# Kernel optimization log

Hardware: AMD Instinct MI355X
Metric: run time of the kernel (lower is better)

Reference implementation:

```python
import jax, jax.numpy as jnp
import numpy as np

N, D = 4096, 512
TAU, ALPHA, BETA = 0.8, 0.55, 0.4
ADJ_P = 0.005  # sparse binary adjacency density (avg degree ~20)


def setup_inputs() -> dict:
    key = jax.random.key(0)
    ks = jax.random.split(key, 8)
    z1 = jax.random.normal(ks[0], (N, D), dtype=jnp.float32)
    z2 = jax.random.normal(ks[1], (N, D), dtype=jnp.float32)

    def adj(k):
        a = jax.random.bernoulli(k, ADJ_P, (N, N)).astype(jnp.float32)
        # adjacency masks are binary {0,1}; zero the diagonal like the model does
        return a * (1.0 - jnp.eye(N, dtype=jnp.float32))

    return {
        "z1": z1,
        "z2": z2,
        "adj_c": adj(ks[2]),
        "adj_m": adj(ks[3]),
        "adj_f": adj(ks[4]),
        "adj_c_aug": adj(ks[5]),
        "adj_m_aug": adj(ks[6]),
        "adj_f_aug": adj(ks[7]),
    }


def _normalize(z):
    # F.normalize(z, dim=1): divide by L2 norm clamped at 1e-12
    n = jnp.maximum(jnp.linalg.norm(z, axis=1, keepdims=True), 1e-12)
    return z / n


def _cl_loss(z, z_aug, adj, tau):
    zn = _normalize(z)
    zan = _normalize(z_aug)
    intra = jnp.exp((zn @ zn.T) / tau)          # [N, N]
    inter = jnp.exp((zn @ zan.T) / tau)         # [N, N]
    intra_diag = jnp.diagonal(intra)
    positive = jnp.diagonal(inter) + (intra * adj).sum(1) + (inter * adj).sum(1)
    denom = intra.sum(1) + inter.sum(1) - intra_diag
    adj_count = adj.sum(1) * 2.0 + 1.0
    loss = jnp.log(positive / denom) / adj_count
    return -jnp.mean(loss)


def _final_cl_loss(z, z_aug, adj, adj_aug, tau):
    return ALPHA * _cl_loss(z, z_aug, adj, tau) + BETA * _cl_loss(z_aug, z, adj_aug, tau)


def reference(z1, z2, adj_c, adj_m, adj_f, adj_c_aug, adj_m_aug, adj_f_aug):
    loss_coarse = _final_cl_loss(z1, z2, adj_c, adj_c_aug, TAU)
    loss_medium = _final_cl_loss(z1, z2, adj_m, adj_m_aug, TAU)
    loss_fine = _final_cl_loss(z1, z2, adj_f, adj_f_aug, TAU)
    loss_cross_cf = _final_cl_loss(z1, z2, adj_c, adj_f_aug, TAU * 0.8)
    loss_cross_mf = _final_cl_loss(z1, z2, adj_m, adj_f_aug, TAU * 0.9)

    sc, sm, sf = adj_c.sum(), adj_m.sum(), adj_f.sum()
    total_info = sc + sm + sf + 1e-08
    scale_loss = (sc / total_info) * loss_coarse + (sm / total_info) * loss_medium + (sf / total_info) * loss_fine
    cross_loss = 0.2 * (loss_cross_cf + loss_cross_mf)
    return scale_loss + cross_loss
```

## Files before the change

kernel.cpp:

```cpp
#include <hip/hip_runtime.h>
#include <hip/hip_bf16.h>

#define NR 4096
#define DD 512
#define CAP 64

typedef __bf16 bf16x8 __attribute__((ext_vector_type(8)));
typedef float f32x4 __attribute__((ext_vector_type(4)));
typedef unsigned short u16;

#define AS_GLOBAL(p) ((const __attribute__((address_space(1))) unsigned int*)(p))
#define AS_LDS(p)    ((__attribute__((address_space(3))) unsigned int*)(p))

__device__ __forceinline__ u16 f2bf(float x) {
    __hip_bfloat16 h = __float2bfloat16(x);
    return *reinterpret_cast<u16*>(&h);
}

__device__ __forceinline__ float blo(unsigned u) { return __uint_as_float(u << 16); }
__device__ __forceinline__ float bhi(unsigned u) { return __uint_as_float(u & 0xffff0000u); }

__global__ void norm_kernel(const float* z1, const float* z2,
                            u16* zn1, u16* zn2, float* d12) {
    const int row = blockIdx.x;
    const int t = threadIdx.x;
    const float* r1 = z1 + (size_t)row * DD;
    const float* r2 = z2 + (size_t)row * DD;
    float a0 = r1[t], a1 = r1[t + 256];
    float b0 = r2[t], b1 = r2[t + 256];
    float ss1 = a0 * a0 + a1 * a1;
    float ss2 = b0 * b0 + b1 * b1;
    #pragma unroll
    for (int m = 1; m < 64; m <<= 1) {
        ss1 += __shfl_xor(ss1, m);
        ss2 += __shfl_xor(ss2, m);
    }
    __shared__ float s1s[4], s2s[4], ds[4];
    const int wid = t >> 6, lane = t & 63;
    if (lane == 0) { s1s[wid] = ss1; s2s[wid] = ss2; }
    __syncthreads();
    const float n1 = s1s[0] + s1s[1] + s1s[2] + s1s[3];
    const float n2 = s2s[0] + s2s[1] + s2s[2] + s2s[3];
    const float inv1 = 1.0f / fmaxf(sqrtf(n1), 1e-12f);
    const float inv2 = 1.0f / fmaxf(sqrtf(n2), 1e-12f);
    const float u0 = a0 * inv1, u1 = a1 * inv1;
    const float v0 = b0 * inv2, v1 = b1 * inv2;
    zn1[(size_t)row * DD + t]       = f2bf(u0);
    zn1[(size_t)row * DD + t + 256] = f2bf(u1);
    zn2[(size_t)row * DD + t]       = f2bf(v0);
    zn2[(size_t)row * DD + t + 256] = f2bf(v1);
    float dp = u0 * v0 + u1 * v1;
    #pragma unroll
    for (int m = 1; m < 64; m <<= 1) dp += __shfl_xor(dp, m);
    if (lane == 0) ds[wid] = dp;
    __syncthreads();
    if (t == 0) d12[row] = ds[0] + ds[1] + ds[2] + ds[3];
}

__global__ __launch_bounds__(256, 2)
void fused_kernel(const u16* __restrict__ zn1, const u16* __restrict__ zn2,
                  const float* __restrict__ m0, const float* __restrict__ m1,
                  const float* __restrict__ m2, const float* __restrict__ m3,
                  const float* __restrict__ m4, const float* __restrict__ m5,
                  float* __restrict__ part, float* __restrict__ ms,
                  float* __restrict__ asum) {
    __shared__ u16 As[128 * 64];
    __shared__ u16 Bs[128 * 64];
    __shared__ float sRow[2][3][128];
    __shared__ float sCol[2][3][128];

    const int bid = blockIdx.x;
    const int tid = threadIdx.x;
    const int lane = tid & 63;

    const float C0 = 1.8033688011112042f;
    const float C1 = 2.2542110013890054f;
    const float C2 = 2.0037431123457825f;

    if ((bid & 3) == 0) {
        int id = bid >> 2;
        int mode, by, bx;
        if (id < 1024) {
            mode = 1; by = id >> 5; bx = id & 31;
        } else {
            int k = id - 1024;
            mode = 0;
            if (k >= 528) { k -= 528; mode = 2; }
            int v = (int)((65.0f - sqrtf(4225.0f - 8.0f * (float)k)) * 0.5f);
            if (v < 0) v = 0; if (v > 31) v = 31;
            while (v < 31 && (v + 1) * 32 - ((v + 1) * v) / 2 <= k) v++;
            while (v > 0 && v * 32 - (v * (v - 1)) / 2 > k) v--;
            by = v;
            bx = by + (k - (by * 32 - (by * (by - 1)) / 2));
        }
        const int Ib = by * 128, Jb = bx * 128;
        const u16* Ag = (mode == 2) ? zn2 : zn1;
        const u16* Bg = (mode == 0) ? zn1 : zn2;
        const int p_row = mode;
        const int p_col = (mode == 1) ? 3 : mode;
        const bool do_cols = (mode == 1) || (bx != by);

        const int wid = tid >> 6;
        const int wm = wid >> 1, wn = wid & 1;
        const int quad = lane >> 4, lcol = lane & 15;

        f32x4 acc[4][4];
        #pragma unroll
        for (int a = 0; a < 4; a++)
            #pragma unroll
            for (int b = 0; b < 4; b++)
                acc[a][b] = (f32x4){0.f, 0.f, 0.f, 0.f};

        size_t gA[4], gB[4];
        unsigned ldsoff[4];
        #pragma unroll
        for (int cc = 0; cc < 4; cc++) {
            const int ch = cc * 4 + wid;
            const int p = ch * 64 + lane;
            const int r = p >> 3;
            const int kb = (p & 7) ^ (r & 7);
            ldsoff[cc] = (unsigned)ch * 1024u;
            gA[cc] = (size_t)(Ib + r) * DD + kb * 8;
            gB[cc] = (size_t)(Jb + r) * DD + kb * 8;
        }

        for (int k0 = 0; k0 < DD; k0 += 64) {
            __syncthreads();
            #pragma unroll
            for (int cc = 0; cc < 4; cc++) {
                __builtin_amdgcn_global_load_lds(AS_GLOBAL(Ag + gA[cc] + k0),
                                                 AS_LDS((char*)As + ldsoff[cc]), 16, 0, 0);
                __builtin_amdgcn_global_load_lds(AS_GLOBAL(Bg + gB[cc] + k0),
                                                 AS_LDS((char*)Bs + ldsoff[cc]), 16, 0, 0);
            }
            __syncthreads();
            #pragma unroll
            for (int kk = 0; kk < 64; kk += 32) {
                const int kbb = (kk >> 3) + quad;
                bf16x8 a[4], b[4];
                #pragma unroll
                for (int i = 0; i < 4; i++) {
                    const int ra = wm * 64 + i * 16 + lcol;
                    const int rb = wn * 64 + i * 16 + lcol;
                    a[i] = *(const bf16x8*)&As[ra * 64 + ((kbb ^ (ra & 7)) * 8)];
                    b[i] = *(const bf16x8*)&Bs[rb * 64 + ((kbb ^ (rb & 7)) * 8)];
                }
                #pragma unroll
                for (int mi = 0; mi < 4; mi++)
                    #pragma unroll
                    for (int ni = 0; ni < 4; ni++)
                        acc[mi][ni] = __builtin_amdgcn_mfma_f32_16x16x32_bf16(a[mi], b[ni], acc[mi][ni], 0, 0, 0);
            }
        }

        float colacc[3][4];
        #pragma unroll
        for (int t = 0; t < 3; t++)
            #pragma unroll
            for (int ni = 0; ni < 4; ni++) colacc[t][ni] = 0.f;

        #pragma unroll
        for (int mi = 0; mi < 4; mi++) {
            #pragma unroll
            for (int reg = 0; reg < 4; reg++) {
                float p0 = 0.f, p1 = 0.f, p2 = 0.f;
                #pragma unroll
                for (int ni = 0; ni < 4; ni++) {
                    const float s = acc[mi][ni][reg];
                    const float e0 = __builtin_amdgcn_exp2f(s * C0);
                    const float e1 = __builtin_amdgcn_exp2f(s * C1);
                    const float e2 = __builtin_amdgcn_exp2f(s * C2);
                    p0 += e0; p1 += e1; p2 += e2;
                    colacc[0][ni] += e0; colacc[1][ni] += e1; colacc[2][ni] += e2;
                }
                p0 += __shfl_xor(p0, 1); p0 += __shfl_xor(p0, 2); p0 += __shfl_xor(p0, 4); p0 += __shfl_xor(p0, 8);
                p1 += __shfl_xor(p1, 1); p1 += __shfl_xor(p1, 2); p1 += __shfl_xor(p1, 4); p1 += __shfl_xor(p1, 8);
                p2 += __shfl_xor(p2, 1); p2 += __shfl_xor(p2, 2); p2 += __shfl_xor(p2, 4); p2 += __shfl_xor(p2, 8);
                if (lcol == 0) {
                    const int r = wm * 64 + mi * 16 + quad * 4 + reg;
                    sRow[wn][0][r] = p0; sRow[wn][1][r] = p1; sRow[wn][2][r] = p2;
                }
            }
        }
        #pragma unroll
        for (int t = 0; t < 3; t++) {
            #pragma unroll
            for (int ni = 0; ni < 4; ni++) {
                float v = colacc[t][ni];
                v += __shfl_xor(v, 16); v += __shfl_xor(v, 32);
                if (quad == 0) sCol[wm][t][wn * 64 + ni * 16 + lcol] = v;
            }
        }
        __syncthreads();
        if (tid < 128) {
            const int i = Ib + tid;
            #pragma unroll
            for (int t = 0; t < 3; t++) {
                const float v = sRow[0][t][tid] + sRow[1][t][tid];
                part[(((size_t)p_row * 3 + t) * 32 + bx) * NR + i] = v;
            }
        } else if (do_cols) {
            const int c = tid - 128;
            const int i = Jb + c;
            #pragma unroll
            for (int t = 0; t < 3; t++) {
                const float v = sCol[0][t][c] + sCol[1][t][c];
                part[(((size_t)p_col * 3 + t) * 32 + by) * NR + i] = v;
            }
        }
    } else {
        const int sid = bid - (bid >> 2) - 1;
        if (sid >= 6144) return;
        const int widx = tid >> 6;
        const int w = sid * 4 + widx;
        const int g = lane >> 4;
        const int l = lane & 15;
        const int m = w >> 12;
        const int i = w & (NR - 1);

        const float* M = (m == 0) ? m0 : (m == 1) ? m1 : (m == 2) ? m2
                       : (m == 3) ? m3 : (m == 4) ? m4 : m5;
        const float4* p = (const float4*)(M + (size_t)i * NR) + lane;
        unsigned long long mask = 0ull;
        #pragma unroll
        for (int t = 0; t < 16; t++) {
            const float4 v = p[t * 64];
            mask |= (unsigned long long)((v.x != 0.f ? 1u : 0u)
                   | (v.y != 0.f ? 2u : 0u)
                   | (v.z != 0.f ? 4u : 0u)
                   | (v.w != 0.f ? 8u : 0u)) << (t * 4);
        }
        const int n = __popcll(mask);
        int off = n;
        #pragma unroll
        for (int d = 1; d < 64; d <<= 1) {
            const int tu = __shfl_up(off, d);
            if (lane >= d) off += tu;
        }
        const int total = __shfl(off, 63);
        int pos = off - n;
        int* lidx = ((int*)As) + widx * 64;
        unsigned long long mm = mask;
        while (mm) {
            const int b = __ffsll(mm) - 1;
            mm &= mm - 1;
            if (pos < CAP) lidx[pos] = ((b >> 2) * 64 + lane) * 4 + (b & 3);
            pos++;
        }
        if (lane == 63) asum[(size_t)m * NR + i] = (float)total;
        const int cnt = min(total, CAP);
        __syncthreads();
        const int jreg = lidx[lane];

        int nslot; int slot[3]; float coef[3];
        switch (m) {
            case 0: nslot = 2; slot[0] = 0; coef[0] = C0; slot[1] = 3; coef[1] = C1; break;
            case 1: nslot = 2; slot[0] = 1; coef[0] = C0; slot[1] = 4; coef[1] = C2; break;
            case 2: nslot = 1; slot[0] = 2; coef[0] = C0; break;
            case 3: nslot = 1; slot[0] = 0; coef[0] = C0; break;
            case 4: nslot = 1; slot[0] = 1; coef[0] = C0; break;
            default: nslot = 3; slot[0] = 2; coef[0] = C0; slot[1] = 3; coef[1] = C1;
                     slot[2] = 4; coef[2] = C2; break;
        }

        const u16* A = (m < 3) ? zn1 : zn2;
        unsigned au[16];
        {
            const uint4* ap = (const uint4*)(A + (size_t)i * DD) + l * 4;
            #pragma unroll
            for (int t = 0; t < 4; t++) {
                const uint4 r = ap[t];
                au[t * 4 + 0] = r.x; au[t * 4 + 1] = r.y;
                au[t * 4 + 2] = r.z; au[t * 4 + 3] = r.w;
            }
        }

        float acc[3][2] = {{0.f, 0.f}, {0.f, 0.f}, {0.f, 0.f}};

        for (int q0 = 0; q0 < cnt; q0 += 8) {
            const int qa = q0 + g;
            const int qb = qa + 4;
            const bool va = qa < cnt;
            const bool vb = qb < cnt;
            const int ja = __shfl(jreg, va ? qa : 0);
            const int jb = __shfl(jreg, vb ? qb : 0);

            const uint4* p1a = (const uint4*)(zn1 + (size_t)ja * DD) + l * 4;
            const uint4* p2a = (const uint4*)(zn2 + (size_t)ja * DD) + l * 4;
            const uint4* p1b = (const uint4*)(zn1 + (size_t)jb * DD) + l * 4;
            const uint4* p2b = (const uint4*)(zn2 + (size_t)jb * DD) + l * 4;
            uint4 r1a[4], r2a[4], r1b[4], r2b[4];
            #pragma unroll
            for (int t = 0; t < 4; t++) {
                r1a[t] = p1a[t]; r2a[t] = p2a[t];
                r1b[t] = p1b[t]; r2b[t] = p2b[t];
            }

            float s1a0 = 0.f, s1a1 = 0.f, s2a0 = 0.f, s2a1 = 0.f;
            float s1b0 = 0.f, s1b1 = 0.f, s2b0 = 0.f, s2b1 = 0.f;
            #pragma unroll
            for (int t = 0; t < 4; t++) {
                const unsigned* u1a = (const unsigned*)&r1a[t];
                const unsigned* u2a = (const unsigned*)&r2a[t];
                const unsigned* u1b = (const unsigned*)&r1b[t];
                const unsigned* u2b = (const unsigned*)&r2b[t];
                #pragma unroll
                for (int q = 0; q < 4; q++) {
                    const unsigned aw = au[t * 4 + q];
                    const float alo = blo(aw), ahi = bhi(aw);
                    s1a0 += alo * blo(u1a[q]); s1a1 += ahi * bhi(u1a[q]);
                    s2a0 += alo * blo(u2a[q]); s2a1 += ahi * bhi(u2a[q]);
                    s1b0 += alo * blo(u1b[q]); s1b1 += ahi * bhi(u1b[q]);
                    s2b0 += alo * blo(u2b[q]); s2b1 += ahi * bhi(u2b[q]);
                }
            }
            float d1a = s1a0 + s1a1, d2a = s2a0 + s2a1;
            float d1b = s1b0 + s1b1, d2b = s2b0 + s2b1;

            #pragma unroll
            for (int msk = 1; msk < 16; msk <<= 1) {
                d1a += __shfl_xor(d1a, msk); d2a += __shfl_xor(d2a, msk);
                d1b += __shfl_xor(d1b, msk); d2b += __shfl_xor(d2b, msk);
            }

            const float e1a = (m < 3) ? d1a : d2a, e2a = (m < 3) ? d2a : d1a;
            const float e1b = (m < 3) ? d1b : d2b, e2b = (m < 3) ? d2b : d1b;
            if (va) {
                for (int s = 0; s < nslot; s++) {
                    acc[s][0] += __builtin_amdgcn_exp2f(e1a * coef[s]);
                    acc[s][1] += __builtin_amdgcn_exp2f(e2a * coef[s]);
                }
            }
            if (vb) {
                for (int s = 0; s < nslot; s++) {
                    acc[s][0] += __builtin_amdgcn_exp2f(e1b * coef[s]);
                    acc[s][1] += __builtin_amdgcn_exp2f(e2b * coef[s]);
                }
            }
        }

        #pragma unroll
        for (int s = 0; s < 3; s++) {
            #pragma unroll
            for (int h = 0; h < 2; h++) {
                float v = acc[s][h];
                v += __shfl_xor(v, 16);
                v += __shfl_xor(v, 32);
                acc[s][h] = v;
            }
        }
        if (lane == 0) {
            const int pb = (m < 3) ? 0 : 2;
            for (int s = 0; s < nslot; s++) {
                ms[((pb)     * 5 + slot[s]) * NR + i] = acc[s][0];
                ms[((pb + 1) * 5 + slot[s]) * NR + i] = acc[s][1];
            }
        }
    }
}

__global__ __launch_bounds__(256)
void reduce_kernel(const float* __restrict__ part, float* __restrict__ rs) {
    const int g = blockIdx.x * 256 + threadIdx.x;
    const int pt = g >> 12;
    const int i = g & (NR - 1);
    const float* base = part + ((size_t)pt * 32) * NR + i;
    float s = 0.f;
    #pragma unroll
    for (int k = 0; k < 32; k++) s += base[(size_t)k * NR];
    rs[(size_t)pt * NR + i] = s;
}

__global__ void finalize_kernel(const float* rs, const float* ms, const float* asum,
                                const float* d12, float* out) {
    const int t = threadIdx.x;
    const int tA[5] = {0, 0, 0, 1, 2};
    const int kA[5] = {0, 1, 2, 3, 4};
    const int aA[5] = {0, 1, 2, 0, 1};
    const int aB[5] = {3, 4, 5, 5, 5};
    const float it[3] = {1.25f, 1.5625f, 1.3888888888888888f};
    const float e1t[3] = {expf(1.25f), expf(1.5625f), expf(1.3888888888888888f)};

    float LA[5] = {0, 0, 0, 0, 0}, LB[5] = {0, 0, 0, 0, 0};
    float sc = 0.f, sm = 0.f, sf = 0.f;

    for (int i = t; i < NR; i += 256) {
        const float d = d12[i];
        float ed[3];
        ed[0] = __expf(d * it[0]); ed[1] = __expf(d * it[1]); ed[2] = __expf(d * it[2]);
        float R[4][3], M[4][5], A6[6];
        #pragma unroll
        for (int p = 0; p < 4; p++) {
            #pragma unroll
            for (int tt = 0; tt < 3; tt++) R[p][tt] = rs[(p * 3 + tt) * NR + i];
            #pragma unroll
            for (int k = 0; k < 5; k++) M[p][k] = ms[(p * 5 + k) * NR + i];
        }
        #pragma unroll
        for (int a = 0; a < 6; a++) A6[a] = asum[a * NR + i];

        #pragma unroll
        for (int c = 0; c < 5; c++) {
            const int tt = tA[c], k = kA[c];
            float pos = ed[tt] + M[0][k] + M[1][k];
            float den = R[0][tt] + R[1][tt] - e1t[tt];
            float cnt = 2.f * A6[aA[c]] + 1.f;
            LA[c] += __logf(pos / den) / cnt;
            pos = ed[tt] + M[2][k] + M[3][k];
            den = R[2][tt] + R[3][tt] - e1t[tt];
            cnt = 2.f * A6[aB[c]] + 1.f;
            LB[c] += __logf(pos / den) / cnt;
        }
        sc += A6[0]; sm += A6[1]; sf += A6[2];
    }

    __shared__ float red[256];
    float vals[13] = {LA[0], LA[1], LA[2], LA[3], LA[4],
                      LB[0], LB[1], LB[2], LB[3], LB[4], sc, sm, sf};
    __shared__ float tot[13];
    for (int q = 0; q < 13; q++) {
        red[t] = vals[q];
        __syncthreads();
        for (int s = 128; s > 0; s >>= 1) {
            if (t < s) red[t] += red[t + s];
            __syncthreads();
        }
        if (t == 0) tot[q] = red[0];
        __syncthreads();
    }
    if (t == 0) {
        float Ac[5], Bc[5];
        #pragma unroll
        for (int c = 0; c < 5; c++) {
            Ac[c] = -tot[c] / (float)NR;
            Bc[c] = -tot[5 + c] / (float)NR;
        }
        const float ALPHA = 0.55f, BETA = 0.4f;
        const float Lc  = ALPHA * Ac[0] + BETA * Bc[0];
        const float Lm  = ALPHA * Ac[1] + BETA * Bc[1];
        const float Lf  = ALPHA * Ac[2] + BETA * Bc[2];
        const float Lcf = ALPHA * Ac[3] + BETA * Bc[3];
        const float Lmf = ALPHA * Ac[4] + BETA * Bc[4];
        const float scs = tot[10], sms = tot[11], sfs = tot[12];
        const float tot_info = scs + sms + sfs + 1e-8f;
        out[0] = (scs * Lc + sms * Lm + sfs * Lf) / tot_info + 0.2f * (Lcf + Lmf);
    }
}

extern "C" void kernel_launch(void* const* d_in, const int* in_sizes, int n_in,
                              void* d_out, int out_size, void* d_ws, size_t ws_size,
                              hipStream_t stream) {
    const float* z1  = (const float*)d_in[0];
    const float* z2  = (const float*)d_in[1];
    const float* ac  = (const float*)d_in[2];
    const float* am  = (const float*)d_in[3];
    const float* af  = (const float*)d_in[4];
    const float* aca = (const float*)d_in[5];
    const float* ama = (const float*)d_in[6];
    const float* afa = (const float*)d_in[7];

    float* ws   = (float*)d_ws;
    float* rs   = ws;
    float* ms   = rs + 12 * NR;
    float* asum = ms + 20 * NR;
    float* d12  = asum + 6 * NR;
    u16* zn1 = (u16*)(d12 + NR);
    u16* zn2 = zn1 + (size_t)NR * DD;
    float* part = (float*)(zn2 + (size_t)NR * DD);

    norm_kernel<<<NR, 256, 0, stream>>>(z1, z2, zn1, zn2, d12);
    fused_kernel<<<8320, 256, 0, stream>>>(zn1, zn2, ac, am, af, aca, ama, afa,
                                           part, ms, asum);
    reduce_kernel<<<12 * NR / 256, 256, 0, stream>>>(part, rs);
    finalize_kernel<<<1, 256, 0, stream>>>(rs, ms, asum, d12, (float*)d_out);
}
```

Measured before the change: 534.1 us.

## Share A tile across two B operands per GEMM block with triangular tiling

Each GEMM block now loads one A tile and two B tiles (zn1 and zn2), computing both the intra and inter similarity tiles in one pass over upper-triangular tile pairs. The inter products are covered by transposed column sums, and the sRow/sCol scratch reuses the A tile's LDS. This cuts A-tile loads and block count from 2080 to 1056 GEMM blocks, and the interleave ratio with the sparse-mask blocks changes from 1:3 to 1:6. It doubles accumulator registers to 128 floats, which may cause spills or lower occupancy under launch_bounds(256,2).

```diff
diff --git a/kernel.cpp b/kernel.cpp
--- a/kernel.cpp
+++ b/kernel.cpp
@@ -65,9 +65,8 @@
                   float* __restrict__ part, float* __restrict__ ms,
                   float* __restrict__ asum) {
     __shared__ u16 As[128 * 64];
-    __shared__ u16 Bs[128 * 64];
-    __shared__ float sRow[2][3][128];
-    __shared__ float sCol[2][3][128];
+    __shared__ u16 Bs1[128 * 64];
+    __shared__ u16 Bs2[128 * 64];
 
     const int bid = blockIdx.x;
     const int tid = threadIdx.x;
@@ -77,39 +76,40 @@
     const float C1 = 2.2542110013890054f;
     const float C2 = 2.0037431123457825f;
 
-    if ((bid & 3) == 0) {
-        int id = bid >> 2;
-        int mode, by, bx;
-        if (id < 1024) {
-            mode = 1; by = id >> 5; bx = id & 31;
-        } else {
-            int k = id - 1024;
-            mode = 0;
-            if (k >= 528) { k -= 528; mode = 2; }
-            int v = (int)((65.0f - sqrtf(4225.0f - 8.0f * (float)k)) * 0.5f);
-            if (v < 0) v = 0; if (v > 31) v = 31;
-            while (v < 31 && (v + 1) * 32 - ((v + 1) * v) / 2 <= k) v++;
-            while (v > 0 && v * 32 - (v * (v - 1)) / 2 > k) v--;
-            by = v;
-            bx = by + (k - (by * 32 - (by * (by - 1)) / 2));
-        }
+    const int q7 = bid / 7;
+    if (bid - q7 * 7 == 0) {
+        const int id = q7;
+        const int grp = id & 1;
+        int k = id >> 1;
+        int v = (int)((65.0f - sqrtf(4225.0f - 8.0f * (float)k)) * 0.5f);
+        if (v < 0) v = 0; if (v > 31) v = 31;
+        while (v < 31 && (v + 1) * 32 - ((v + 1) * v) / 2 <= k) v++;
+        while (v > 0 && v * 32 - (v * (v - 1)) / 2 > k) v--;
+        const int by = v;
+        const int bx = by + (k - (by * 32 - (by * (by - 1)) / 2));
+
         const int Ib = by * 128, Jb = bx * 128;
-        const u16* Ag = (mode == 2) ? zn2 : zn1;
-        const u16* Bg = (mode == 0) ? zn1 : zn2;
-        const int p_row = mode;
-        const int p_col = (mode == 1) ? 3 : mode;
-        const bool do_cols = (mode == 1) || (bx != by);
+        const bool diag = (bx == by);
+        const u16* Ag  = grp ? zn2 : zn1;
+        const u16* B1g = grp ? zn2 : zn1;
+        const u16* B2g = grp ? zn1 : zn2;
+        const bool dualB = !(grp == 1 && diag);
+        const int pR1 = grp ? 2 : 0;
+        const int pR2 = grp ? 3 : 1;
+        const int pC2 = grp ? 1 : 3;
 
         const int wid = tid >> 6;
         const int wm = wid >> 1, wn = wid & 1;
         const int quad = lane >> 4, lcol = lane & 15;
 
-        f32x4 acc[4][4];
+        f32x4 acc1[4][4], acc2[4][4];
         #pragma unroll
         for (int a = 0; a < 4; a++)
             #pragma unroll
-            for (int b = 0; b < 4; b++)
-                acc[a][b] = (f32x4){0.f, 0.f, 0.f, 0.f};
+            for (int b = 0; b < 4; b++) {
+                acc1[a][b] = (f32x4){0.f, 0.f, 0.f, 0.f};
+                acc2[a][b] = (f32x4){0.f, 0.f, 0.f, 0.f};
+            }
 
         size_t gA[4], gB[4];
         unsigned ldsoff[4];
@@ -130,55 +130,86 @@
             for (int cc = 0; cc < 4; cc++) {
                 __builtin_amdgcn_global_load_lds(AS_GLOBAL(Ag + gA[cc] + k0),
                                                  AS_LDS((char*)As + ldsoff[cc]), 16, 0, 0);
-                __builtin_amdgcn_global_load_lds(AS_GLOBAL(Bg + gB[cc] + k0),
-                                                 AS_LDS((char*)Bs + ldsoff[cc]), 16, 0, 0);
+                __builtin_amdgcn_global_load_lds(AS_GLOBAL(B1g + gB[cc] + k0),
+                                                 AS_LDS((char*)Bs1 + ldsoff[cc]), 16, 0, 0);
+                if (dualB)
+                    __builtin_amdgcn_global_load_lds(AS_GLOBAL(B2g + gB[cc] + k0),
+                                                     AS_LDS((char*)Bs2 + ldsoff[cc]), 16, 0, 0);
             }
             __syncthreads();
             #pragma unroll
             for (int kk = 0; kk < 64; kk += 32) {
                 const int kbb = (kk >> 3) + quad;
-                bf16x8 a[4], b[4];
+                bf16x8 a[4], b1[4], b2[4];
                 #pragma unroll
                 for (int i = 0; i < 4; i++) {
                     const int ra = wm * 64 + i * 16 + lcol;
                     const int rb = wn * 64 + i * 16 + lcol;
-                    a[i] = *(const bf16x8*)&As[ra * 64 + ((kbb ^ (ra & 7)) * 8)];
-                    b[i] = *(const bf16x8*)&Bs[rb * 64 + ((kbb ^ (rb & 7)) * 8)];
+                    a[i]  = *(const bf16x8*)&As[ra * 64 + ((kbb ^ (ra & 7)) * 8)];
+                    b1[i] = *(const bf16x8*)&Bs1[rb * 64 + ((kbb ^ (rb & 7)) * 8)];
+                    if (dualB)
+                        b2[i] = *(const bf16x8*)&Bs2[rb * 64 + ((kbb ^ (rb & 7)) * 8)];
                 }
                 #pragma unroll
                 for (int mi = 0; mi < 4; mi++)
                     #pragma unroll
-                    for (int ni = 0; ni < 4; ni++)
-                        acc[mi][ni] = __builtin_amdgcn_mfma_f32_16x16x32_bf16(a[mi], b[ni], acc[mi][ni], 0, 0, 0);
-            }
-        }
-
-        float colacc[3][4];
+                    for (int ni = 0; ni < 4; ni++) {
+                        acc1[mi][ni] = __builtin_amdgcn_mfma_f32_16x16x32_bf16(a[mi], b1[ni], acc1[mi][ni], 0, 0, 0);
+                        if (dualB)
+                            acc2[mi][ni] = __builtin_amdgcn_mfma_f32_16x16x32_bf16(a[mi], b2[ni], acc2[mi][ni], 0, 0, 0);
+                    }
+            }
+        }
+
+        float* eb = (float*)As;
+        float* sRow1 = eb;
+        float* sRow2 = eb + 768;
+        float* sCol1 = eb + 1536;
+        float* sCol2 = eb + 2304;
+        __syncthreads();
+
+        float ca1[3][4], ca2[3][4];
         #pragma unroll
         for (int t = 0; t < 3; t++)
             #pragma unroll
-            for (int ni = 0; ni < 4; ni++) colacc[t][ni] = 0.f;
+            for (int ni = 0; ni < 4; ni++) { ca1[t][ni] = 0.f; ca2[t][ni] = 0.f; }
 
         #pragma unroll
         for (int mi = 0; mi < 4; mi++) {
             #pragma unroll
             for (int reg = 0; reg < 4; reg++) {
-                float p0 = 0.f, p1 = 0.f, p2 = 0.f;
+                float p10 = 0.f, p11 = 0.f, p12 = 0.f;
+                float p20 = 0.f, p21 = 0.f, p22 = 0.f;
                 #pragma unroll
                 for (int ni = 0; ni < 4; ni++) {
-                    const float s = acc[mi][ni][reg];
-                    const float e0 = __builtin_amdgcn_exp2f(s * C0);
-                    const float e1 = __builtin_amdgcn_exp2f(s * C1);
-                    const float e2 = __builtin_amdgcn_exp2f(s * C2);
-                    p0 += e0; p1 += e1; p2 += e2;
-                    colacc[0][ni] += e0; colacc[1][ni] += e1; colacc[2][ni] += e2;
-                }
-                p0 += __shfl_xor(p0, 1); p0 += __shfl_xor(p0, 2); p0 += __shfl_xor(p0, 4); p0 += __shfl_xor(p0, 8);
-                p1 += __shfl_xor(p1, 1); p1 += __shfl_xor(p1, 2); p1 += __shfl_xor(p1, 4); p1 += __shfl_xor(p1, 8);
-                p2 += __shfl_xor(p2, 1); p2 += __shfl_xor(p2, 2); p2 += __shfl_xor(p2, 4); p2 += __shfl_xor(p2, 8);
+                    const float s1 = acc1[mi][ni][reg];
+                    const float e0 = __builtin_amdgcn_exp2f(s1 * C0);
+                    const float e1 = __builtin_amdgcn_exp2f(s1 * C1);
+                    const float e2 = __builtin_amdgcn_exp2f(s1 * C2);
+                    p10 += e0; p11 += e1; p12 += e2;
+                    ca1[0][ni] += e0; ca1[1][ni] += e1; ca1[2][ni] += e2;
+                    if (dualB) {
+                        const float s2 = acc2[mi][ni][reg];
+                        const float f0 = __builtin_amdgcn_exp2f(s2 * C0);
+                        const float f1 = __builtin_amdgcn_exp2f(s2 * C1);
+                        const float f2 = __builtin_amdgcn_exp2f(s2 * C2);
+                        p20 += f0; p21 += f1; p22 += f2;
+                        ca2[0][ni] += f0; ca2[1][ni] += f1; ca2[2][ni] += f2;
+                    }
+                }
+                #pragma unroll
+                for (int msk = 1; msk < 16; msk <<= 1) {
+                    p10 += __shfl_xor(p10, msk); p11 += __shfl_xor(p11, msk); p12 += __shfl_xor(p12, msk);
+                    p20 += __shfl_xor(p20, msk); p21 += __shfl_xor(p21, msk); p22 += __shfl_xor(p22, msk);
+                }
                 if (lcol == 0) {
                     const int r = wm * 64 + mi * 16 + quad * 4 + reg;
-                    sRow[wn][0][r] = p0; sRow[wn][1][r] = p1; sRow[wn][2][r] = p2;
+                    sRow1[wn * 384 + 0 * 128 + r] = p10;
+                    sRow1[wn * 384 + 1 * 128 + r] = p11;
+                    sRow1[wn * 384 + 2 * 128 + r] = p12;
+                    sRow2[wn * 384 + 0 * 128 + r] = p20;
+                    sRow2[wn * 384 + 1 * 128 + r] = p21;
+                    sRow2[wn * 384 + 2 * 128 + r] = p22;
                 }
             }
         }
@@ -186,9 +217,14 @@
         for (int t = 0; t < 3; t++) {
             #pragma unroll
             for (int ni = 0; ni < 4; ni++) {
-                float v = colacc[t][ni];
-                v += __shfl_xor(v, 16); v += __shfl_xor(v, 32);
-                if (quad == 0) sCol[wm][t][wn * 64 + ni * 16 + lcol] = v;
+                float v1 = ca1[t][ni], v2 = ca2[t][ni];
+                v1 += __shfl_xor(v1, 16); v1 += __shfl_xor(v1, 32);
+                v2 += __shfl_xor(v2, 16); v2 += __shfl_xor(v2, 32);
+                if (quad == 0) {
+                    const int c = wn * 64 + ni * 16 + lcol;
+                    sCol1[wm * 384 + t * 128 + c] = v1;
+                    sCol2[wm * 384 + t * 128 + c] = v2;
+                }
             }
         }
         __syncthreads();
@@ -196,20 +232,30 @@
             const int i = Ib + tid;
             #pragma unroll
             for (int t = 0; t < 3; t++) {
-                const float v = sRow[0][t][tid] + sRow[1][t][tid];
-                part[(((size_t)p_row * 3 + t) * 32 + bx) * NR + i] = v;
-            }
-        } else if (do_cols) {
+                const float r1 = sRow1[t * 128 + tid] + sRow1[384 + t * 128 + tid];
+                part[(((size_t)pR1 * 3 + t) * 32 + bx) * NR + i] = r1;
+                if (dualB) {
+                    const float r2 = sRow2[t * 128 + tid] + sRow2[384 + t * 128 + tid];
+                    part[(((size_t)pR2 * 3 + t) * 32 + bx) * NR + i] = r2;
+                }
+            }
+        } else {
             const int c = tid - 128;
-            const int i = Jb + c;
+            const int j = Jb + c;
             #pragma unroll
             for (int t = 0; t < 3; t++) {
-                const float v = sCol[0][t][c] + sCol[1][t][c];
-                part[(((size_t)p_col * 3 + t) * 32 + by) * NR + i] = v;
+                if (!diag) {
+                    const float c1 = sCol1[t * 128 + c] + sCol1[384 + t * 128 + c];
+                    part[(((size_t)pR1 * 3 + t) * 32 + by) * NR + j] = c1;
+                }
+                if (dualB) {
+                    const float c2 = sCol2[t * 128 + c] + sCol2[384 + t * 128 + c];
+                    part[(((size_t)pC2 * 3 + t) * 32 + by) * NR + j] = c2;
+                }
             }
         }
     } else {
-        const int sid = bid - (bid >> 2) - 1;
+        const int sid = bid - q7 - 1;
         if (sid >= 6144) return;
         const int widx = tid >> 6;
         const int w = sid * 4 + widx;
@@ -343,10 +389,10 @@
         for (int s = 0; s < 3; s++) {
             #pragma unroll
             for (int h = 0; h < 2; h++) {
-                float v = acc[s][h];
-                v += __shfl_xor(v, 16);
-                v += __shfl_xor(v, 32);
-                acc[s][h] = v;
+                float v2 = acc[s][h];
+                v2 += __shfl_xor(v2, 16);
+                v2 += __shfl_xor(v2, 32);
+                acc[s][h] = v2;
             }
         }
         if (lane == 0) {
@@ -469,7 +515,7 @@
     float* part = (float*)(zn2 + (size_t)NR * DD);
 
     norm_kernel<<<NR, 256, 0, stream>>>(z1, z2, zn1, zn2, d12);
-    fused_kernel<<<8320, 256, 0, stream>>>(zn1, zn2, ac, am, af, aca, ama, afa,
+    fused_kernel<<<7392, 256, 0, stream>>>(zn1, zn2, ac, am, af, aca, ama, afa,
                                            part, ms, asum);
     reduce_kernel<<<12 * NR / 256, 256, 0, stream>>>(part, rs);
     finalize_kernel<<<1, 256, 0, stream>>>(rs, ms, asum, d12, (float*)d_out);
```

Measured after the change: 521.1 us. -2.4%, faster.

## Rebalance fused kernel: 2 GEMM per 3 sparse blocks, two rows per wave, more occupancy

Applied to the files above, without the earlier changes.

Changes the block interleave from one GEMM tile per four blocks to two GEMM tiles per five blocks. Each sparse wave now scans two adjacency rows at once and processes neighbors one per 16-lane group instead of two. The epilogue's row and column scratch now reuses the As shared buffer, which cuts LDS so launch bounds can ask for three blocks per SM. Aims to raise occupancy and overlap the HBM-bound mask scan with the MFMA tiles, at the cost of more register pressure and less per-wave memory-level parallelism in the gather loop.

```diff
diff --git a/kernel.cpp b/kernel.cpp
--- a/kernel.cpp
+++ b/kernel.cpp
@@ -57,7 +57,7 @@
     if (t == 0) d12[row] = ds[0] + ds[1] + ds[2] + ds[3];
 }
 
-__global__ __launch_bounds__(256, 2)
+__global__ __launch_bounds__(256, 3)
 void fused_kernel(const u16* __restrict__ zn1, const u16* __restrict__ zn2,
                   const float* __restrict__ m0, const float* __restrict__ m1,
                   const float* __restrict__ m2, const float* __restrict__ m3,
@@ -66,8 +66,6 @@
                   float* __restrict__ asum) {
     __shared__ u16 As[128 * 64];
     __shared__ u16 Bs[128 * 64];
-    __shared__ float sRow[2][3][128];
-    __shared__ float sCol[2][3][128];
 
     const int bid = blockIdx.x;
     const int tid = threadIdx.x;
@@ -77,8 +75,11 @@
     const float C1 = 2.2542110013890054f;
     const float C2 = 2.0037431123457825f;
 
-    if ((bid & 3) == 0) {
-        int id = bid >> 2;
+    const int g5 = bid / 5;
+    const int r5 = bid - g5 * 5;
+
+    if (r5 < 2) {
+        const int id = g5 * 2 + r5;
         int mode, by, bx;
         if (id < 1024) {
             mode = 1; by = id >> 5; bx = id & 31;
@@ -153,6 +154,11 @@
             }
         }
 
+        __syncthreads();
+        float* eb = (float*)As;
+        float* sRow = eb;
+        float* sCol = eb + 768;
+
         float colacc[3][4];
         #pragma unroll
         for (int t = 0; t < 3; t++)
@@ -173,12 +179,17 @@
                     p0 += e0; p1 += e1; p2 += e2;
                     colacc[0][ni] += e0; colacc[1][ni] += e1; colacc[2][ni] += e2;
                 }
-                p0 += __shfl_xor(p0, 1); p0 += __shfl_xor(p0, 2); p0 += __shfl_xor(p0, 4); p0 += __shfl_xor(p0, 8);
-                p1 += __shfl_xor(p1, 1); p1 += __shfl_xor(p1, 2); p1 += __shfl_xor(p1, 4); p1 += __shfl_xor(p1, 8);
-                p2 += __shfl_xor(p2, 1); p2 += __shfl_xor(p2, 2); p2 += __shfl_xor(p2, 4); p2 += __shfl_xor(p2, 8);
+                #pragma unroll
+                for (int msk = 1; msk < 16; msk <<= 1) {
+                    p0 += __shfl_xor(p0, msk);
+                    p1 += __shfl_xor(p1, msk);
+                    p2 += __shfl_xor(p2, msk);
+                }
                 if (lcol == 0) {
                     const int r = wm * 64 + mi * 16 + quad * 4 + reg;
-                    sRow[wn][0][r] = p0; sRow[wn][1][r] = p1; sRow[wn][2][r] = p2;
+                    sRow[wn * 384 + 0 * 128 + r] = p0;
+                    sRow[wn * 384 + 1 * 128 + r] = p1;
+                    sRow[wn * 384 + 2 * 128 + r] = p2;
                 }
             }
         }
@@ -188,7 +199,7 @@
             for (int ni = 0; ni < 4; ni++) {
                 float v = colacc[t][ni];
                 v += __shfl_xor(v, 16); v += __shfl_xor(v, 32);
-                if (quad == 0) sCol[wm][t][wn * 64 + ni * 16 + lcol] = v;
+                if (quad == 0) sCol[wm * 384 + t * 128 + wn * 64 + ni * 16 + lcol] = v;
             }
         }
         __syncthreads();
@@ -196,61 +207,80 @@
             const int i = Ib + tid;
             #pragma unroll
             for (int t = 0; t < 3; t++) {
-                const float v = sRow[0][t][tid] + sRow[1][t][tid];
+                const float v = sRow[t * 128 + tid] + sRow[384 + t * 128 + tid];
                 part[(((size_t)p_row * 3 + t) * 32 + bx) * NR + i] = v;
             }
         } else if (do_cols) {
             const int c = tid - 128;
-            const int i = Jb + c;
+            const int j = Jb + c;
             #pragma unroll
             for (int t = 0; t < 3; t++) {
-                const float v = sCol[0][t][c] + sCol[1][t][c];
-                part[(((size_t)p_col * 3 + t) * 32 + by) * NR + i] = v;
+                const float v = sCol[t * 128 + c] + sCol[384 + t * 128 + c];
+                part[(((size_t)p_col * 3 + t) * 32 + by) * NR + j] = v;
             }
         }
     } else {
-        const int sid = bid - (bid >> 2) - 1;
-        if (sid >= 6144) return;
+        const int sid = g5 * 3 + (r5 - 2);
+        if (sid >= 3072) return;
         const int widx = tid >> 6;
-        const int w = sid * 4 + widx;
-        const int g = lane >> 4;
+        const int grp = lane >> 4;
         const int l = lane & 15;
-        const int m = w >> 12;
-        const int i = w & (NR - 1);
+        const int wbase = sid * 8 + widx * 2;
+        const int m = wbase >> 12;
+        const int i0 = wbase & (NR - 1);
 
         const float* M = (m == 0) ? m0 : (m == 1) ? m1 : (m == 2) ? m2
                        : (m == 3) ? m3 : (m == 4) ? m4 : m5;
-        const float4* p = (const float4*)(M + (size_t)i * NR) + lane;
-        unsigned long long mask = 0ull;
+        const float4* p0 = (const float4*)(M + (size_t)i0 * NR) + lane;
+        const float4* p1 = (const float4*)(M + (size_t)(i0 + 1) * NR) + lane;
+        unsigned long long mask0 = 0ull, mask1 = 0ull;
         #pragma unroll
         for (int t = 0; t < 16; t++) {
-            const float4 v = p[t * 64];
-            mask |= (unsigned long long)((v.x != 0.f ? 1u : 0u)
-                   | (v.y != 0.f ? 2u : 0u)
-                   | (v.z != 0.f ? 4u : 0u)
-                   | (v.w != 0.f ? 8u : 0u)) << (t * 4);
-        }
-        const int n = __popcll(mask);
-        int off = n;
+            const float4 va = p0[t * 64];
+            const float4 vb = p1[t * 64];
+            mask0 |= (unsigned long long)((va.x != 0.f ? 1u : 0u)
+                   | (va.y != 0.f ? 2u : 0u)
+                   | (va.z != 0.f ? 4u : 0u)
+                   | (va.w != 0.f ? 8u : 0u)) << (t * 4);
+            mask1 |= (unsigned long long)((vb.x != 0.f ? 1u : 0u)
+                   | (vb.y != 0.f ? 2u : 0u)
+                   | (vb.z != 0.f ? 4u : 0u)
+                   | (vb.w != 0.f ? 8u : 0u)) << (t * 4);
+        }
+        const int n0 = __popcll(mask0), n1 = __popcll(mask1);
+        int off0 = n0, off1 = n1;
         #pragma unroll
         for (int d = 1; d < 64; d <<= 1) {
-            const int tu = __shfl_up(off, d);
-            if (lane >= d) off += tu;
-        }
-        const int total = __shfl(off, 63);
-        int pos = off - n;
-        int* lidx = ((int*)As) + widx * 64;
-        unsigned long long mm = mask;
+            const int t0 = __shfl_up(off0, d);
+            const int t1 = __shfl_up(off1, d);
+            if (lane >= d) { off0 += t0; off1 += t1; }
+        }
+        const int total0 = __shfl(off0, 63), total1 = __shfl(off1, 63);
+        int* lidx0 = ((int*)As) + widx * 128;
+        int* lidx1 = lidx0 + 64;
+        int pos = off0 - n0;
+        unsigned long long mm = mask0;
         while (mm) {
             const int b = __ffsll(mm) - 1;
             mm &= mm - 1;
-            if (pos < CAP) lidx[pos] = ((b >> 2) * 64 + lane) * 4 + (b & 3);
+            if (pos < CAP) lidx0[pos] = ((b >> 2) * 64 + lane) * 4 + (b & 3);
             pos++;
         }
-        if (lane == 63) asum[(size_t)m * NR + i] = (float)total;
-        const int cnt = min(total, CAP);
-        __syncthreads();
-        const int jreg = lidx[lane];
+        pos = off1 - n1;
+        mm = mask1;
+        while (mm) {
+            const int b = __ffsll(mm) - 1;
+            mm &= mm - 1;
+            if (pos < CAP) lidx1[pos] = ((b >> 2) * 64 + lane) * 4 + (b & 3);
+            pos++;
+        }
+        if (lane == 63) {
+            asum[(size_t)m * NR + i0]     = (float)total0;
+            asum[(size_t)m * NR + i0 + 1] = (float)total1;
+        }
+        const int cnt0 = min(total0, CAP), cnt1 = min(total1, CAP);
+        const int jreg0 = lidx0[lane];
+        const int jreg1 = lidx1[lane];
 
         int nslot; int slot[3]; float coef[3];
         switch (m) {
@@ -264,96 +294,81 @@
         }
 
         const u16* A = (m < 3) ? zn1 : zn2;
-        unsigned au[16];
-        {
-            const uint4* ap = (const uint4*)(A + (size_t)i * DD) + l * 4;
-            #pragma unroll
-            for (int t = 0; t < 4; t++) {
-                const uint4 r = ap[t];
-                au[t * 4 + 0] = r.x; au[t * 4 + 1] = r.y;
-                au[t * 4 + 2] = r.z; au[t * 4 + 3] = r.w;
-            }
-        }
-
-        float acc[3][2] = {{0.f, 0.f}, {0.f, 0.f}, {0.f, 0.f}};
-
-        for (int q0 = 0; q0 < cnt; q0 += 8) {
-            const int qa = q0 + g;
-            const int qb = qa + 4;
-            const bool va = qa < cnt;
-            const bool vb = qb < cnt;
-            const int ja = __shfl(jreg, va ? qa : 0);
-            const int jb = __shfl(jreg, vb ? qb : 0);
-
-            const uint4* p1a = (const uint4*)(zn1 + (size_t)ja * DD) + l * 4;
-            const uint4* p2a = (const uint4*)(zn2 + (size_t)ja * DD) + l * 4;
-            const uint4* p1b = (const uint4*)(zn1 + (size_t)jb * DD) + l * 4;
-            const uint4* p2b = (const uint4*)(zn2 + (size_t)jb * DD) + l * 4;
-            uint4 r1a[4], r2a[4], r1b[4], r2b[4];
-            #pragma unroll
-            for (int t = 0; t < 4; t++) {
-                r1a[t] = p1a[t]; r2a[t] = p2a[t];
-                r1b[t] = p1b[t]; r2b[t] = p2b[t];
-            }
-
-            float s1a0 = 0.f, s1a1 = 0.f, s2a0 = 0.f, s2a1 = 0.f;
-            float s1b0 = 0.f, s1b1 = 0.f, s2b0 = 0.f, s2b1 = 0.f;
-            #pragma unroll
-            for (int t = 0; t < 4; t++) {
-                const unsigned* u1a = (const unsigned*)&r1a[t];
-                const unsigned* u2a = (const unsigned*)&r2a[t];
-                const unsigned* u1b = (const unsigned*)&r1b[t];
-                const unsigned* u2b = (const unsigned*)&r2b[t];
-                #pragma unroll
-                for (int q = 0; q < 4; q++) {
-                    const unsigned aw = au[t * 4 + q];
-                    const float alo = blo(aw), ahi = bhi(aw);
-                    s1a0 += alo * blo(u1a[q]); s1a1 += ahi * bhi(u1a[q]);
-                    s2a0 += alo * blo(u2a[q]); s2a1 += ahi * bhi(u2a[q]);
-                    s1b0 += alo * blo(u1b[q]); s1b1 += ahi * bhi(u1b[q]);
-                    s2b0 += alo * blo(u2b[q]); s2b1 += ahi * bhi(u2b[q]);
-                }
-            }
-            float d1a = s1a0 + s1a1, d2a = s2a0 + s2a1;
-            float d1b = s1b0 + s1b1, d2b = s2b0 + s2b1;
-
-            #pragma unroll
-            for (int msk = 1; msk < 16; msk <<= 1) {
-                d1a += __shfl_xor(d1a, msk); d2a += __shfl_xor(d2a, msk);
-                d1b += __shfl_xor(d1b, msk); d2b += __shfl_xor(d2b, msk);
-            }
-
-            const float e1a = (m < 3) ? d1a : d2a, e2a = (m < 3) ? d2a : d1a;
-            const float e1b = (m < 3) ? d1b : d2b, e2b = (m < 3) ? d2b : d1b;
-            if (va) {
+
+        for (int rr = 0; rr < 2; rr++) {
+            const int i = i0 + rr;
+            const int cnt = rr ? cnt1 : cnt0;
+            const int jreg = rr ? jreg1 : jreg0;
+
+            unsigned au[16];
+            {
+                const uint4* ap = (const uint4*)(A + (size_t)i * DD) + l * 4;
+                #pragma unroll
+                for (int t = 0; t < 4; t++) {
+                    const uint4 r = ap[t];
+                    au[t * 4 + 0] = r.x; au[t * 4 + 1] = r.y;
+                    au[t * 4 + 2] = r.z; au[t * 4 + 3] = r.w;
+                }
+            }
+
+            float acc[3][2] = {{0.f, 0.f}, {0.f, 0.f}, {0.f, 0.f}};
+
+            for (int q0 = 0; q0 < cnt; q0 += 4) {
+                const int q = q0 + grp;
+                const bool valid = q < cnt;
+                const int j = __shfl(jreg, valid ? q : 0);
+
+                const uint4* pj1 = (const uint4*)(zn1 + (size_t)j * DD) + l * 4;
+                const uint4* pj2 = (const uint4*)(zn2 + (size_t)j * DD) + l * 4;
+                uint4 r1[4], r2[4];
+                #pragma unroll
+                for (int t = 0; t < 4; t++) { r1[t] = pj1[t]; r2[t] = pj2[t]; }
+
+                float s10 = 0.f, s11 = 0.f, s20 = 0.f, s21 = 0.f;
+                #pragma unroll
+                for (int t = 0; t < 4; t++) {
+                    const unsigned* u1 = (const unsigned*)&r1[t];
+                    const unsigned* u2 = (const unsigned*)&r2[t];
+                    #pragma unroll
+                    for (int qd = 0; qd < 4; qd++) {
+                        const unsigned aw = au[t * 4 + qd];
+                        const float alo = blo(aw), ahi = bhi(aw);
+                        s10 += alo * blo(u1[qd]); s11 += ahi * bhi(u1[qd]);
+                        s20 += alo * blo(u2[qd]); s21 += ahi * bhi(u2[qd]);
+                    }
+                }
+                float d1 = s10 + s11, d2 = s20 + s21;
+                #pragma unroll
+                for (int msk = 1; msk < 16; msk <<= 1) {
+                    d1 += __shfl_xor(d1, msk);
+                    d2 += __shfl_xor(d2, msk);
+                }
+                const float e1 = (m < 3) ? d1 : d2;
+                const float e2 = (m < 3) ? d2 : d1;
+                if (valid) {
+                    for (int s = 0; s < nslot; s++) {
+                        acc[s][0] += __builtin_amdgcn_exp2f(e1 * coef[s]);
+                        acc[s][1] += __builtin_amdgcn_exp2f(e2 * coef[s]);
+                    }
+                }
+            }
+
+            #pragma unroll
+            for (int s = 0; s < 3; s++) {
+                #pragma unroll
+                for (int h = 0; h < 2; h++) {
+                    float v = acc[s][h];
+                    v += __shfl_xor(v, 16);
+                    v += __shfl_xor(v, 32);
+                    acc[s][h] = v;
+                }
+            }
+            if (lane == 0) {
+                const int pb = (m < 3) ? 0 : 2;
                 for (int s = 0; s < nslot; s++) {
-                    acc[s][0] += __builtin_amdgcn_exp2f(e1a * coef[s]);
-                    acc[s][1] += __builtin_amdgcn_exp2f(e2a * coef[s]);
-                }
-            }
-            if (vb) {
-                for (int s = 0; s < nslot; s++) {
-                    acc[s][0] += __builtin_amdgcn_exp2f(e1b * coef[s]);
-                    acc[s][1] += __builtin_amdgcn_exp2f(e2b * coef[s]);
-                }
-            }
-        }
-
-        #pragma unroll
-        for (int s = 0; s < 3; s++) {
-            #pragma unroll
-            for (int h = 0; h < 2; h++) {
-                float v = acc[s][h];
-                v += __shfl_xor(v, 16);
-                v += __shfl_xor(v, 32);
-                acc[s][h] = v;
-            }
-        }
-        if (lane == 0) {
-            const int pb = (m < 3) ? 0 : 2;
-            for (int s = 0; s < nslot; s++) {
-                ms[((pb)     * 5 + slot[s]) * NR + i] = acc[s][0];
-                ms[((pb + 1) * 5 + slot[s]) * NR + i] = acc[s][1];
+                    ms[((pb)     * 5 + slot[s]) * NR + i] = acc[s][0];
+                    ms[((pb + 1) * 5 + slot[s]) * NR + i] = acc[s][1];
+                }
             }
         }
     }
@@ -469,7 +484,7 @@
     float* part = (float*)(zn2 + (size_t)NR * DD);
 
     norm_kernel<<<NR, 256, 0, stream>>>(z1, z2, zn1, zn2, d12);
-    fused_kernel<<<8320, 256, 0, stream>>>(zn1, zn2, ac, am, af, aca, ama, afa,
+    fused_kernel<<<5200, 256, 0, stream>>>(zn1, zn2, ac, am, af, aca, ama, afa,
                                            part, ms, asum);
     reduce_kernel<<<12 * NR / 256, 256, 0, stream>>>(part, rs);
     finalize_kernel<<<1, 256, 0, stream>>>(rs, ms, asum, d12, (float*)d_out);
```

Measured after the change: 512.0 us. -4.2%, faster.
